# Performance work log

Measured on AMD Instinct MI355X. Metric: run time of the kernel, lower is better.

The kernel has to match this reference:

```python
import jax, jax.numpy as jnp
import numpy as np
from math import sqrt

E = 1024          # embedding_size
A = 64            # attention_size (per-head)
H = E // A        # 16 heads
FF = 4 * E        # 4096
B, S = 2, 2048
EPS = 1e-5


def layernorm(x, g, b):
    mu = jnp.mean(x, axis=-1, keepdims=True)
    var = jnp.mean(jnp.square(x - mu), axis=-1, keepdims=True)
    return (x - mu) * jax.lax.rsqrt(var + EPS) * g + b


def setup_inputs() -> dict:
    key = jax.random.key(0)
    ks = jax.random.split(key, 12)
    s = 0.02
    return {
        "embedding": jax.random.normal(ks[0], (B, S, E), jnp.float32),
        "positional_encoding": jax.random.normal(ks[1], (B, S, E), jnp.float32),
        # per-head QKV projections (no bias), stacked over heads: [H, E, A]
        "Wq": jax.random.normal(ks[2], (H, E, A), jnp.float32) * s,
        "Wk": jax.random.normal(ks[3], (H, E, A), jnp.float32) * s,
        "Wv": jax.random.normal(ks[4], (H, E, A), jnp.float32) * s,
        "Wproj": jax.random.normal(ks[5], (E, E), jnp.float32) * s,  # no bias
        "W1": jax.random.normal(ks[6], (E, FF), jnp.float32) * s,
        "b1": jnp.zeros((FF,), jnp.float32),
        "W2": jax.random.normal(ks[7], (FF, E), jnp.float32) * s,
        "b2": jnp.zeros((E,), jnp.float32),
        # LayerNorm params: attn norm, FFN-internal norm, final FF norm
        "g_attn": jnp.ones((E,), jnp.float32), "be_attn": jnp.zeros((E,), jnp.float32),
        "g_ffn": jnp.ones((E,), jnp.float32), "be_ffn": jnp.zeros((E,), jnp.float32),
        "g_out": jnp.ones((E,), jnp.float32), "be_out": jnp.zeros((E,), jnp.float32),
    }


def reference(embedding, positional_encoding, Wq, Wk, Wv, Wproj, W1, b1, W2, b2,
              g_attn, be_attn, g_ffn, be_ffn, g_out, be_out):
    x = embedding + positional_encoding                       # [B,S,E]
    # All heads at once (original loops over heads; same math):
    Q = jnp.einsum('bse,hea->hbsa', x, Wq)                    # [H,B,S,A]
    K = jnp.einsum('bse,hea->hbsa', x, Wk)
    V = jnp.einsum('bse,hea->hbsa', x, Wv)
    # NOTE: original scales by sqrt(input dim) = sqrt(E), not sqrt(A)
    scale = sqrt(E)
    scores = jnp.einsum('hbsa,hbta->hbst', Q, K) / scale      # [H,B,S,S]
    causal = jnp.tril(jnp.ones((S, S), bool))                 # j >= k allowed
    scores = jnp.where(causal, scores, -jnp.inf)
    probs = jax.nn.softmax(scores, axis=-1)
    attn = jnp.einsum('hbst,hbta->hbsa', probs, V)            # [H,B,S,A]
    # concat heads along feature dim -> [B,S,H*A] = [B,S,E]
    attn = jnp.transpose(attn, (1, 2, 0, 3)).reshape(x.shape[0], x.shape[1], E)
    attn = attn @ Wproj                                       # linear proj, no bias
    mha = layernorm(x + attn, g_attn, be_attn)
    # FeedForward: relu applied AFTER the second linear (as in source)
    hidden = mha @ W1 + b1
    ff = jax.nn.relu(hidden @ W2 + b2)
    ff_out = layernorm(mha + ff, g_ffn, be_ffn)
    encoded = layernorm(mha + ff_out, g_out, be_out)
    return encoded, K, V
```

## Files before the change

kernel.cpp:

```cpp
#include <hip/hip_runtime.h>


typedef unsigned short u16;
typedef unsigned int u32;
typedef __bf16 bf16x8 __attribute__((ext_vector_type(8)));
typedef float f32x4 __attribute__((ext_vector_type(4)));

#define AS1 __attribute__((address_space(1)))
#define AS3 __attribute__((address_space(3)))

__device__ __forceinline__ u16 f2bf(float f) {
    u32 x = __float_as_uint(f);
    x += 0x7fffu + ((x >> 16) & 1u);
    return (u16)(x >> 16);
}

__device__ __forceinline__ int swz(int row) { return ((row ^ (row >> 2)) & 7) << 4; }

__device__ __forceinline__ void gload16(void* lds, const void* g) {
    __builtin_amdgcn_global_load_lds((const AS1 void*)(unsigned long long)g,
                                     (AS3 void*)(u32)(unsigned long long)lds, 16, 0, 0);
}

template <int BM, int AMODE, int OMODE>
__launch_bounds__(256, 3)
__global__ void k_mm(const void* Ap, const u16* __restrict__ Bt, int K, int KZ,
                     float* C, float* Cp, const float* __restrict__ bias,
                     const float* resid, const float* resid2,
                     u16* oQb, float* oKf, u16* oKb, float* oVf, int relu) {
    constexpr int MF = BM / 32;
    __shared__ __align__(16) u16 As[BM * 64];
    __shared__ __align__(16) u16 Bs[128 * 64];
    const int tid = threadIdx.x;
    const int wave = tid >> 6, lane = tid & 63, quad = lane >> 4, l16 = lane & 15;
    const int wm = wave & 1, wn = wave >> 1;
    const int m0 = blockIdx.x * BM, n0 = blockIdx.y * 128;
    const int kbeg = blockIdx.z * KZ, kend = kbeg + KZ;

    f32x4 acc[MF][4];
#pragma unroll
    for (int mf = 0; mf < MF; ++mf)
#pragma unroll
        for (int nf = 0; nf < 4; ++nf) acc[mf][nf] = (f32x4){0.f, 0.f, 0.f, 0.f};

    for (int kk = kbeg; kk < kend; kk += 64) {
        __syncthreads();
        if constexpr (AMODE == 1) {
            const float* Af = (const float*)Ap;
#pragma unroll
            for (int i = 0; i < BM / 16; ++i) {
                const int slot = tid + i * 256;
                const int row = slot >> 4, c4 = (slot & 15) * 4;
                float4 v = *(const float4*)(Af + (long long)(m0 + row) * K + kk + c4);
                ushort4 s;
                s.x = f2bf(v.x); s.y = f2bf(v.y); s.z = f2bf(v.z); s.w = f2bf(v.w);
                *(ushort4*)((char*)As + row * 128 + ((c4 * 2) ^ swz(row))) = s;
            }
        } else {
            const u16* Ab = (const u16*)Ap;
#pragma unroll
            for (int i = 0; i < BM / 32; ++i) {
                const int chunk = wave * (BM / 32) + i;
                const int row = chunk * 8 + (lane >> 3);
                const int cb = (lane & 7) * 16;
                const int e = kk + ((cb ^ swz(row)) >> 1);
                const u16* src;
                if constexpr (AMODE == 2)
                    src = Ab + (long long)(e >> 6) * 262144 + (long long)(m0 + row) * 64 + (e & 63);
                else
                    src = Ab + (long long)(m0 + row) * K + e;
                gload16((char*)As + chunk * 1024, src);
            }
        }
#pragma unroll
        for (int i = 0; i < 4; ++i) {
            const int chunk = wave * 4 + i;
            const int row = chunk * 8 + (lane >> 3);
            const int cb = (lane & 7) * 16;
            gload16((char*)Bs + chunk * 1024,
                    Bt + (long long)(n0 + row) * K + kk + ((cb ^ swz(row)) >> 1));
        }
        __syncthreads();
#pragma unroll
        for (int ks = 0; ks < 2; ++ks) {
            bf16x8 af[MF], bfr[4];
#pragma unroll
            for (int mf = 0; mf < MF; ++mf) {
                const int row = wm * (BM / 2) + mf * 16 + l16;
                af[mf] = *(const bf16x8*)((const char*)As + row * 128 +
                                          ((ks * 64 + quad * 16) ^ swz(row)));
            }
#pragma unroll
            for (int nf = 0; nf < 4; ++nf) {
                const int row = wn * 64 + nf * 16 + l16;
                bfr[nf] = *(const bf16x8*)((const char*)Bs + row * 128 +
                                           ((ks * 64 + quad * 16) ^ swz(row)));
            }
#pragma unroll
            for (int mf = 0; mf < MF; ++mf)
#pragma unroll
                for (int nf = 0; nf < 4; ++nf)
                    acc[mf][nf] = __builtin_amdgcn_mfma_f32_16x16x32_bf16(af[mf], bfr[nf],
                                                                          acc[mf][nf], 0, 0, 0);
        }
    }

#pragma unroll
    for (int mf = 0; mf < MF; ++mf) {
#pragma unroll
        for (int nf = 0; nf < 4; ++nf) {
#pragma unroll
            for (int r = 0; r < 4; ++r) {
                const long long row = m0 + wm * (BM / 2) + mf * 16 + quad * 4 + r;
                const int col = n0 + wn * 64 + nf * 16 + l16;
                float v = acc[mf][nf][r];
                if constexpr (OMODE == 0) {
                    if (bias) v += bias[col];
                    if (relu) v = fmaxf(v, 0.f);
                    if (resid) v += resid[row * 1024 + col];
                    if (resid2) v += resid2[row * 1024 + col];
                    C[row * 1024 + col] = v;
                } else if constexpr (OMODE == 1) {
                    const int sel = col >> 10, h = (col >> 6) & 15, a = col & 63;
                    const long long idx = (long long)h * 262144 + row * 64 + a;
                    if (sel == 0) oQb[idx] = f2bf(v);
                    else if (sel == 1) { oKf[idx] = v; oKb[idx] = f2bf(v); }
                    else oVf[idx] = v;
                } else {
                    Cp[(long long)blockIdx.z * 1048576 + (long long)col * 1024 + row] = v;
                }
            }
        }
    }
}

__global__ void k_prep(const float* __restrict__ emb, const float* __restrict__ pos,
                       const float* __restrict__ W1, const float* __restrict__ W2,
                       const float* __restrict__ Wq, const float* __restrict__ Wk,
                       const float* __restrict__ Wv, const float* __restrict__ Wp,
                       const float* __restrict__ b2,
                       u16* __restrict__ xb, u16* __restrict__ W1b,
                       u16* __restrict__ W2t, u16* __restrict__ WBt,
                       u16* __restrict__ WpT, float* __restrict__ b12) {
    __shared__ float T[64][65];
    const int bx = blockIdx.x, tid = threadIdx.x;
    if (bx < 8192) {
        const long long i = ((long long)(bx & 4095) * 256 + tid) * 4;
        const float* a = (bx < 4096) ? emb : W1;
        u16* o = (bx < 4096) ? xb : W1b;
        float4 v = *(const float4*)(a + i);
        if (bx < 4096) {
            float4 u = *(const float4*)(pos + i);
            v.x += u.x; v.y += u.y; v.z += u.z; v.w += u.w;
        }
        ushort4 s;
        s.x = f2bf(v.x); s.y = f2bf(v.y); s.z = f2bf(v.z); s.w = f2bf(v.w);
        *(ushort4*)(o + i) = s;
        return;
    }
    if (bx == 10240) {
        float4 v = *(const float4*)(b2 + tid * 4);
        *(float4*)(b12 + tid * 4) = v;
        return;
    }
    const float* ip;
    u16* op;
    long long ldin, ldout;
    if (bx < 9216) {
        const int t = bx - 8192, x = t & 63, z = t >> 6;
        ip = W2 + (long long)z * 64 + (long long)x * 65536;
        ldin = 1024;
        op = W2t + (long long)z * 262144 + x * 64;
        ldout = 4096;
    } else {
        const int t = bx - 9216, x = t & 15, z = t >> 4;
        const int w = z >> 4, h = z & 15;
        if (w < 3) {
            ip = (w == 0 ? Wq : (w == 1 ? Wk : Wv)) + h * 65536 + x * 4096;
            ldin = 64;
            op = WBt + (long long)(w * 16 + h) * 65536 + x * 64;
        } else {
            ip = Wp + x * 65536 + h * 64;
            ldin = 1024;
            op = WpT + (long long)h * 65536 + x * 64;
        }
        ldout = 1024;
    }
#pragma unroll
    for (int i = 0; i < 4; ++i) {
        const int slot = tid + i * 256;
        const int r = slot >> 4, c4 = (slot & 15) * 4;
        float4 v = *(const float4*)(ip + (long long)r * ldin + c4);
        T[r][c4] = v.x; T[r][c4 + 1] = v.y; T[r][c4 + 2] = v.z; T[r][c4 + 3] = v.w;
    }
    __syncthreads();
#pragma unroll
    for (int i = 0; i < 4; ++i) {
        const int slot = tid + i * 256;
        const int c = slot >> 4, r4 = (slot & 15) * 4;
        ushort4 s;
        s.x = f2bf(T[r4][c]); s.y = f2bf(T[r4 + 1][c]);
        s.z = f2bf(T[r4 + 2][c]); s.w = f2bf(T[r4 + 3][c]);
        *(ushort4*)(op + (long long)c * ldout + r4) = s;
    }
}

__global__ void k_tc(const float* __restrict__ in, u16* __restrict__ out,
                     long long ldin, long long ldout, long long szin, long long szout) {
    __shared__ float T[64][65];
    const int x = blockIdx.x, z = blockIdx.y, tid = threadIdx.x;
    const float* ip = in + (long long)z * szin + (long long)x * 64 * ldin;
    u16* op = out + (long long)z * szout + (long long)x * 64;
#pragma unroll
    for (int i = 0; i < 4; ++i) {
        const int slot = tid + i * 256;
        const int r = slot >> 4, c4 = (slot & 15) * 4;
        float4 v = *(const float4*)(ip + (long long)r * ldin + c4);
        T[r][c4] = v.x; T[r][c4 + 1] = v.y; T[r][c4 + 2] = v.z; T[r][c4 + 3] = v.w;
    }
    __syncthreads();
#pragma unroll
    for (int i = 0; i < 4; ++i) {
        const int slot = tid + i * 256;
        const int c = slot >> 4, r4 = (slot & 15) * 4;
        ushort4 s;
        s.x = f2bf(T[r4][c]); s.y = f2bf(T[r4 + 1][c]);
        s.z = f2bf(T[r4 + 2][c]); s.w = f2bf(T[r4 + 3][c]);
        *(ushort4*)(op + (long long)c * ldout + r4) = s;
    }
}

__global__ void k_rb(const float* __restrict__ P, u16* __restrict__ out,
                     const float* __restrict__ b1, const float* __restrict__ W2,
                     float* __restrict__ b12) {
    const int bx = blockIdx.x, tid = threadIdx.x;
    if (bx < 1024) {
        const long long i = ((long long)bx * 256 + tid) * 4;
        float4 a = *(const float4*)(P + i);
        float4 b = *(const float4*)(P + i + 1048576);
        float4 c = *(const float4*)(P + i + 2097152);
        float4 d = *(const float4*)(P + i + 3145728);
        ushort4 s;
        s.x = f2bf(a.x + b.x + c.x + d.x); s.y = f2bf(a.y + b.y + c.y + d.y);
        s.z = f2bf(a.z + b.z + c.z + d.z); s.w = f2bf(a.w + b.w + c.w + d.w);
        *(ushort4*)(out + i) = s;
    } else {
        const int z = bx - 1024;
        const int o4 = tid * 4;
        const float* Wr = W2 + (long long)z * 16384 + o4;
        float ax = 0.f, ay = 0.f, az = 0.f, aw = 0.f;
#pragma unroll
        for (int ff = 0; ff < 16; ++ff) {
            const float bb = b1[z * 16 + ff];
            float4 w = *(const float4*)(Wr + ff * 1024);
            ax += bb * w.x; ay += bb * w.y; az += bb * w.z; aw += bb * w.w;
        }
        atomicAdd(b12 + o4, ax);
        atomicAdd(b12 + o4 + 1, ay);
        atomicAdd(b12 + o4 + 2, az);
        atomicAdd(b12 + o4 + 3, aw);
    }
}

__launch_bounds__(512, 2)
__global__ void k_flash(u16* Qb, const u16* __restrict__ Kb, const u16* __restrict__ Vg) {
    __shared__ __align__(16) u16 Ks[2][64 * 64];
    __shared__ __align__(16) u16 Vs[2][64 * 64];
    __shared__ __align__(16) u16 Pb[8][16 * 64];
    const int tid = threadIdx.x;
    const int wave = tid >> 6, lane = tid & 63, quad = lane >> 4, l16 = lane & 15;
    const int hb = blockIdx.y, h = hb >> 1, b = hb & 1;
    const int xr = 15 - (int)blockIdx.x;
    const int q0 = xr * 128;
    const long long qbase = (long long)h * 262144 + (long long)b * 131072;
    u16* Qp = Qb + qbase + (long long)q0 * 64;
    const u16* Kp = Kb + qbase;
    const u16* Vp = Vg + (long long)hb * 131072;
    const float NEG = -1.0e30f;

    const int qrow = wave * 16 + l16;
    const bf16x8 aq0 = *(const bf16x8*)(Qp + qrow * 64 + quad * 8);
    const bf16x8 aq1 = *(const bf16x8*)(Qp + qrow * 64 + 32 + quad * 8);

    f32x4 o[4];
#pragma unroll
    for (int g = 0; g < 4; ++g) o[g] = (f32x4){0.f, 0.f, 0.f, 0.f};
    float mrun = NEG, lrun = 0.f;
    u16* Pw = Pb[wave];

    auto stage = [&](int bi, int k0) {
        const int row = tid >> 3;
        const int cb = (tid & 7) * 16;
        const int eo = (cb ^ swz(row)) >> 1;
        gload16((char*)Ks[bi] + tid * 16, Kp + (long long)(k0 + row) * 64 + eo);
        gload16((char*)Vs[bi] + tid * 16, Vp + (long long)row * 2048 + k0 + eo);
    };

    const int nit = 2 * xr + 2;
    stage(0, 0);
    int cur = 0;
    for (int it = 0; it < nit; ++it) {
        __syncthreads();
        if (it + 1 < nit) stage(cur ^ 1, (it + 1) * 64);
        f32x4 sc[4];
        __builtin_amdgcn_s_setprio(1);
#pragma unroll
        for (int kg = 0; kg < 4; ++kg) {
            const int krow = kg * 16 + l16;
            const bf16x8 bka = *(const bf16x8*)((const char*)Ks[cur] + krow * 128 +
                                                ((quad * 16) ^ swz(krow)));
            const bf16x8 bkb = *(const bf16x8*)((const char*)Ks[cur] + krow * 128 +
                                                ((64 + quad * 16) ^ swz(krow)));
            sc[kg] = (f32x4){0.f, 0.f, 0.f, 0.f};
            sc[kg] = __builtin_amdgcn_mfma_f32_16x16x32_bf16(bka, aq0, sc[kg], 0, 0, 0);
            sc[kg] = __builtin_amdgcn_mfma_f32_16x16x32_bf16(bkb, aq1, sc[kg], 0, 0, 0);
        }
        __builtin_amdgcn_s_setprio(0);
        const int k0 = it * 64;
        const int q = q0 + wave * 16 + l16;
        const bool edge = (it >= nit - 2);
        float vv[4][4];
        float tmax = NEG;
#pragma unroll
        for (int kg = 0; kg < 4; ++kg)
#pragma unroll
            for (int r = 0; r < 4; ++r) {
                float x = sc[kg][r] * 0.03125f;
                if (edge && (k0 + kg * 16 + quad * 4 + r > q)) x = NEG;
                vv[kg][r] = x;
                tmax = fmaxf(tmax, x);
            }
        tmax = fmaxf(tmax, __shfl_xor(tmax, 16));
        tmax = fmaxf(tmax, __shfl_xor(tmax, 32));
        if (__all(tmax - mrun <= 8.f)) {
            float rs = 0.f;
#pragma unroll
            for (int kg = 0; kg < 4; ++kg)
#pragma unroll
                for (int r = 0; r < 4; ++r) {
                    const float e = __expf(vv[kg][r] - mrun);
                    vv[kg][r] = e;
                    rs += e;
                }
            rs += __shfl_xor(rs, 16);
            rs += __shfl_xor(rs, 32);
            lrun += rs;
        } else {
            const float mn = fmaxf(mrun, tmax);
            const float alpha = __expf(mrun - mn);
            mrun = mn;
            float rs = 0.f;
#pragma unroll
            for (int kg = 0; kg < 4; ++kg)
#pragma unroll
                for (int r = 0; r < 4; ++r) {
                    const float e = __expf(vv[kg][r] - mn);
                    vv[kg][r] = e;
                    rs += e;
                }
            rs += __shfl_xor(rs, 16);
            rs += __shfl_xor(rs, 32);
            lrun = lrun * alpha + rs;
#pragma unroll
            for (int r = 0; r < 4; ++r) {
                const float ar = __shfl(alpha, quad * 4 + r, 16);
#pragma unroll
                for (int g = 0; g < 4; ++g) o[g][r] *= ar;
            }
        }
#pragma unroll
        for (int kg = 0; kg < 4; ++kg) {
            ushort4 s;
            s.x = f2bf(vv[kg][0]); s.y = f2bf(vv[kg][1]);
            s.z = f2bf(vv[kg][2]); s.w = f2bf(vv[kg][3]);
            *(ushort4*)((char*)Pw + l16 * 128 + ((kg * 32 + quad * 8) ^ swz(l16))) = s;
        }
        const bf16x8 ap0 = *(const bf16x8*)((const char*)Pw + l16 * 128 +
                                            ((quad * 16) ^ swz(l16)));
        const bf16x8 ap1 = *(const bf16x8*)((const char*)Pw + l16 * 128 +
                                            ((64 + quad * 16) ^ swz(l16)));
        __builtin_amdgcn_s_setprio(1);
#pragma unroll
        for (int g = 0; g < 4; ++g) {
            const int ar = g * 16 + l16;
            const bf16x8 bv0 = *(const bf16x8*)((const char*)Vs[cur] + ar * 128 +
                                                ((quad * 16) ^ swz(ar)));
            const bf16x8 bv1 = *(const bf16x8*)((const char*)Vs[cur] + ar * 128 +
                                                ((64 + quad * 16) ^ swz(ar)));
            o[g] = __builtin_amdgcn_mfma_f32_16x16x32_bf16(ap0, bv0, o[g], 0, 0, 0);
            o[g] = __builtin_amdgcn_mfma_f32_16x16x32_bf16(ap1, bv1, o[g], 0, 0, 0);
        }
        __builtin_amdgcn_s_setprio(0);
        cur ^= 1;
    }

#pragma unroll
    for (int r = 0; r < 4; ++r) {
        const float lr = __shfl(lrun, quad * 4 + r, 16);
        const float inv = 1.0f / lr;
        const int srow = wave * 16 + quad * 4 + r;
#pragma unroll
        for (int g = 0; g < 4; ++g)
            Qp[srow * 64 + g * 16 + l16] = f2bf(o[g][r] * inv);
    }
}

__global__ void k_ln(const float* in1, const float* in2,
                     const float* __restrict__ g, const float* __restrict__ be,
                     float* out) {
    __shared__ float red[8];
    const int m = blockIdx.x, tid = threadIdx.x, e0 = tid * 4;
    const long long bp = (long long)m * 1024;
    float4 v = *(const float4*)(in1 + bp + e0);
    if (in2) {
        float4 u = *(const float4*)(in2 + bp + e0);
        v.x += u.x; v.y += u.y; v.z += u.z; v.w += u.w;
    }
    float s1 = v.x + v.y + v.z + v.w;
    float s2 = v.x * v.x + v.y * v.y + v.z * v.z + v.w * v.w;
#pragma unroll
    for (int off = 1; off < 64; off <<= 1) { s1 += __shfl_xor(s1, off); s2 += __shfl_xor(s2, off); }
    if ((tid & 63) == 0) { red[tid >> 6] = s1; red[4 + (tid >> 6)] = s2; }
    __syncthreads();
    const float S1 = red[0] + red[1] + red[2] + red[3];
    const float S2 = red[4] + red[5] + red[6] + red[7];
    const float mean = S1 * (1.0f / 1024.0f);
    const float var = S2 * (1.0f / 1024.0f) - mean * mean;
    const float rstd = rsqrtf(var + 1e-5f);
    float4 ug = *(const float4*)(g + e0);
    float4 ub = *(const float4*)(be + e0);
    float4 o;
    o.x = (v.x - mean) * rstd * ug.x + ub.x;
    o.y = (v.y - mean) * rstd * ug.y + ub.y;
    o.z = (v.z - mean) * rstd * ug.z + ub.z;
    o.w = (v.w - mean) * rstd * ug.w + ub.w;
    *(float4*)(out + bp + e0) = o;
}

__global__ void k_ln23(const float* r2, const float* __restrict__ mha,
                       const float* __restrict__ g1, const float* __restrict__ be1,
                       const float* __restrict__ g2, const float* __restrict__ be2,
                       float* out) {
    __shared__ float red[8];
    const int m = blockIdx.x, tid = threadIdx.x, e0 = tid * 4;
    const long long bp = (long long)m * 1024;
    float4 v = *(const float4*)(r2 + bp + e0);
    float s1 = v.x + v.y + v.z + v.w;
    float s2 = v.x * v.x + v.y * v.y + v.z * v.z + v.w * v.w;
#pragma unroll
    for (int off = 1; off < 64; off <<= 1) { s1 += __shfl_xor(s1, off); s2 += __shfl_xor(s2, off); }
    if ((tid & 63) == 0) { red[tid >> 6] = s1; red[4 + (tid >> 6)] = s2; }
    __syncthreads();
    float S1 = red[0] + red[1] + red[2] + red[3];
    float S2 = red[4] + red[5] + red[6] + red[7];
    float mean = S1 * (1.0f / 1024.0f);
    float rstd = rsqrtf(S2 * (1.0f / 1024.0f) - mean * mean + 1e-5f);
    float4 ug = *(const float4*)(g1 + e0);
    float4 ub = *(const float4*)(be1 + e0);
    float4 vm = *(const float4*)(mha + bp + e0);
    float4 t;
    t.x = vm.x + (v.x - mean) * rstd * ug.x + ub.x;
    t.y = vm.y + (v.y - mean) * rstd * ug.y + ub.y;
    t.z = vm.z + (v.z - mean) * rstd * ug.z + ub.z;
    t.w = vm.w + (v.w - mean) * rstd * ug.w + ub.w;
    s1 = t.x + t.y + t.z + t.w;
    s2 = t.x * t.x + t.y * t.y + t.z * t.z + t.w * t.w;
#pragma unroll
    for (int off = 1; off < 64; off <<= 1) { s1 += __shfl_xor(s1, off); s2 += __shfl_xor(s2, off); }
    __syncthreads();
    if ((tid & 63) == 0) { red[tid >> 6] = s1; red[4 + (tid >> 6)] = s2; }
    __syncthreads();
    S1 = red[0] + red[1] + red[2] + red[3];
    S2 = red[4] + red[5] + red[6] + red[7];
    mean = S1 * (1.0f / 1024.0f);
    rstd = rsqrtf(S2 * (1.0f / 1024.0f) - mean * mean + 1e-5f);
    ug = *(const float4*)(g2 + e0);
    ub = *(const float4*)(be2 + e0);
    float4 oo;
    oo.x = (t.x - mean) * rstd * ug.x + ub.x;
    oo.y = (t.y - mean) * rstd * ug.y + ub.y;
    oo.z = (t.z - mean) * rstd * ug.z + ub.z;
    oo.w = (t.w - mean) * rstd * ug.w + ub.w;
    *(float4*)(out + bp + e0) = oo;
}

extern "C" void kernel_launch(void* const* d_in, const int* in_sizes, int n_in,
                              void* d_out, int out_size, void* d_ws, size_t ws_size,
                              hipStream_t stream) {
    (void)in_sizes; (void)n_in; (void)out_size; (void)ws_size;
    const float* emb    = (const float*)d_in[0];
    const float* pos    = (const float*)d_in[1];
    const float* Wq     = (const float*)d_in[2];
    const float* Wk     = (const float*)d_in[3];
    const float* Wv     = (const float*)d_in[4];
    const float* Wproj  = (const float*)d_in[5];
    const float* W1     = (const float*)d_in[6];
    const float* b1     = (const float*)d_in[7];
    const float* W2     = (const float*)d_in[8];
    const float* b2     = (const float*)d_in[9];
    const float* g_attn = (const float*)d_in[10];
    const float* be_attn= (const float*)d_in[11];
    const float* g_ffn  = (const float*)d_in[12];
    const float* be_ffn = (const float*)d_in[13];
    const float* g_out  = (const float*)d_in[14];
    const float* be_out = (const float*)d_in[15];

    float* enc   = (float*)d_out;
    float* out_K = enc + 4194304;
    float* out_V = enc + 8388608;
    u16* QbU  = (u16*)enc;
    u16* KbU  = (u16*)enc + 4194304;
    u16* W1b  = (u16*)enc;
    u16* W2t  = (u16*)enc + 4194304;
    float* Ppart = out_K;

    u16* wsu    = (u16*)d_ws;
    u16* WBt    = wsu;
    u16* xb     = wsu + 4194304;
    u16* VbT    = wsu;
    u16* WpT    = wsu + 8388608;
    u16* W12T   = wsu + 9437184;
    float* b12  = (float*)(wsu + 10485760);
    float* res1 = (float*)d_ws;

    k_prep<<<10241, 256, 0, stream>>>(emb, pos, W1, W2, Wq, Wk, Wv, Wproj, b2,
                                      xb, W1b, W2t, WBt, WpT, b12);
    k_mm<64, 0, 2><<<dim3(16, 8, 4), 256, 0, stream>>>(W1b, W2t, 4096, 1024,
        nullptr, Ppart, nullptr, nullptr, nullptr, nullptr, nullptr, nullptr, nullptr, 0);
    k_rb<<<1280, 256, 0, stream>>>(Ppart, W12T, b1, W2, b12);

    k_mm<128, 0, 1><<<dim3(32, 24), 256, 0, stream>>>(xb, WBt, 1024, 1024,
        nullptr, nullptr, nullptr, nullptr, nullptr, QbU, out_K, KbU, out_V, 0);
    k_tc<<<dim3(32, 32), 256, 0, stream>>>(out_V, VbT, 64, 2048, 131072, 131072);

    k_flash<<<dim3(16, 32), 512, 0, stream>>>(QbU, KbU, VbT);

    k_mm<64, 2, 0><<<dim3(64, 8), 256, 0, stream>>>(QbU, WpT, 1024, 1024,
        res1, nullptr, nullptr, emb, pos, nullptr, nullptr, nullptr, nullptr, 0);
    k_ln<<<4096, 256, 0, stream>>>(res1, nullptr, g_attn, be_attn, res1);

    k_mm<64, 1, 0><<<dim3(64, 8), 256, 0, stream>>>(res1, W12T, 1024, 1024,
        enc, nullptr, b12, res1, nullptr, nullptr, nullptr, nullptr, nullptr, 1);
    k_ln23<<<4096, 256, 0, stream>>>(enc, res1, g_ffn, be_ffn, g_out, be_out, enc);
}
```

Before: 387.5 us.

## Double-buffer LDS tiles in GEMM kernel to overlap loads with MFMA

```diff
diff --git a/kernel.cpp b/kernel.cpp
--- a/kernel.cpp
+++ b/kernel.cpp
@@ -10,9 +10,7 @@
 #define AS3 __attribute__((address_space(3)))
 
 __device__ __forceinline__ u16 f2bf(float f) {
-    u32 x = __float_as_uint(f);
-    x += 0x7fffu + ((x >> 16) & 1u);
-    return (u16)(x >> 16);
+    return __builtin_bit_cast(u16, static_cast<__bf16>(f));
 }
 
 __device__ __forceinline__ int swz(int row) { return ((row ^ (row >> 2)) & 7) << 4; }
@@ -23,19 +21,20 @@
 }
 
 template <int BM, int AMODE, int OMODE>
-__launch_bounds__(256, 3)
+__launch_bounds__(256, (BM == 128) ? 2 : 3)
 __global__ void k_mm(const void* Ap, const u16* __restrict__ Bt, int K, int KZ,
                      float* C, float* Cp, const float* __restrict__ bias,
                      const float* resid, const float* resid2,
                      u16* oQb, float* oKf, u16* oKb, float* oVf, int relu) {
     constexpr int MF = BM / 32;
-    __shared__ __align__(16) u16 As[BM * 64];
-    __shared__ __align__(16) u16 Bs[128 * 64];
+    __shared__ __align__(16) u16 As[2][BM * 64];
+    __shared__ __align__(16) u16 Bs[2][128 * 64];
     const int tid = threadIdx.x;
     const int wave = tid >> 6, lane = tid & 63, quad = lane >> 4, l16 = lane & 15;
     const int wm = wave & 1, wn = wave >> 1;
     const int m0 = blockIdx.x * BM, n0 = blockIdx.y * 128;
-    const int kbeg = blockIdx.z * KZ, kend = kbeg + KZ;
+    const int kbeg = blockIdx.z * KZ;
+    const int nk = KZ / 64;
 
     f32x4 acc[MF][4];
 #pragma unroll
@@ -43,8 +42,7 @@
 #pragma unroll
         for (int nf = 0; nf < 4; ++nf) acc[mf][nf] = (f32x4){0.f, 0.f, 0.f, 0.f};
 
-    for (int kk = kbeg; kk < kend; kk += 64) {
-        __syncthreads();
+    auto stageA = [&](int b, int kk) {
         if constexpr (AMODE == 1) {
             const float* Af = (const float*)Ap;
 #pragma unroll
@@ -54,7 +52,7 @@
                 float4 v = *(const float4*)(Af + (long long)(m0 + row) * K + kk + c4);
                 ushort4 s;
                 s.x = f2bf(v.x); s.y = f2bf(v.y); s.z = f2bf(v.z); s.w = f2bf(v.w);
-                *(ushort4*)((char*)As + row * 128 + ((c4 * 2) ^ swz(row))) = s;
+                *(ushort4*)((char*)As[b] + row * 128 + ((c4 * 2) ^ swz(row))) = s;
             }
         } else {
             const u16* Ab = (const u16*)Ap;
@@ -69,31 +67,43 @@
                     src = Ab + (long long)(e >> 6) * 262144 + (long long)(m0 + row) * 64 + (e & 63);
                 else
                     src = Ab + (long long)(m0 + row) * K + e;
-                gload16((char*)As + chunk * 1024, src);
-            }
-        }
+                gload16((char*)As[b] + chunk * 1024, src);
+            }
+        }
+    };
+    auto stageB = [&](int b, int kk) {
 #pragma unroll
         for (int i = 0; i < 4; ++i) {
             const int chunk = wave * 4 + i;
             const int row = chunk * 8 + (lane >> 3);
             const int cb = (lane & 7) * 16;
-            gload16((char*)Bs + chunk * 1024,
+            gload16((char*)Bs[b] + chunk * 1024,
                     Bt + (long long)(n0 + row) * K + kk + ((cb ^ swz(row)) >> 1));
         }
+    };
+
+    stageA(0, kbeg);
+    stageB(0, kbeg);
+    int cur = 0;
+    for (int t = 0; t < nk; ++t) {
         __syncthreads();
+        if (t + 1 < nk) {
+            stageA(cur ^ 1, kbeg + (t + 1) * 64);
+            stageB(cur ^ 1, kbeg + (t + 1) * 64);
+        }
 #pragma unroll
         for (int ks = 0; ks < 2; ++ks) {
             bf16x8 af[MF], bfr[4];
 #pragma unroll
             for (int mf = 0; mf < MF; ++mf) {
                 const int row = wm * (BM / 2) + mf * 16 + l16;
-                af[mf] = *(const bf16x8*)((const char*)As + row * 128 +
+                af[mf] = *(const bf16x8*)((const char*)As[cur] + row * 128 +
                                           ((ks * 64 + quad * 16) ^ swz(row)));
             }
 #pragma unroll
             for (int nf = 0; nf < 4; ++nf) {
                 const int row = wn * 64 + nf * 16 + l16;
-                bfr[nf] = *(const bf16x8*)((const char*)Bs + row * 128 +
+                bfr[nf] = *(const bf16x8*)((const char*)Bs[cur] + row * 128 +
                                            ((ks * 64 + quad * 16) ^ swz(row)));
             }
 #pragma unroll
@@ -103,6 +113,7 @@
                     acc[mf][nf] = __builtin_amdgcn_mfma_f32_16x16x32_bf16(af[mf], bfr[nf],
                                                                           acc[mf][nf], 0, 0, 0);
         }
+        cur ^= 1;
     }
 
 #pragma unroll
```

New measurement: 364.7 us. 5.9% less time.
